# Kernel optimization log

Hardware: AMD Instinct MI355X
Metric: run time of the kernel (lower is better)

## Reference

```python
import jax, jax.numpy as jnp
import numpy as np

B, H, S, D = 4, 32, 2048, 128  # batch, heads, seq_len, d_head
D_MODEL = H * D


def setup_inputs() -> dict:
    key = jax.random.key(0)
    ks = jax.random.split(key, 6)
    return {
        "query_states": jax.random.normal(ks[0], (B, H, S, D), dtype=jnp.float32),
        "key_states": jax.random.normal(ks[1], (B, H, S, D), dtype=jnp.float32),
        "value_states": jax.random.normal(ks[2], (B, H, S, D), dtype=jnp.float32),
        "local_attn_outputs": jax.random.normal(ks[3], (B, H, S, D), dtype=jnp.float32),
        "balance_factors": jax.random.normal(ks[4], (H,), dtype=jnp.float32),
        "w_o": jax.random.normal(ks[5], (D_MODEL, D_MODEL), dtype=jnp.float32) / np.sqrt(D_MODEL),
    }


def reference(query_states, key_states, value_states, local_attn_outputs, balance_factors, w_o):
    # --- compressive memory from keys/values (elu+1 feature map) ---
    phi_k = jax.nn.elu(key_states) + 1.0                                  # [B,H,S,D]
    memory = jnp.einsum("bhsk,bhsv->bhkv", phi_k, value_states)           # [B,H,D,D]
    normalization = jnp.sum(phi_k, axis=2)                                # [B,H,D]

    # --- retrieval with query feature map, normalized ---
    phi_q = jax.nn.elu(query_states) + 1.0                                # [B,H,S,D]
    retrieved = jnp.einsum("bhsk,bhkv->bhsv", phi_q, memory)              # [B,H,S,D]
    denom = jnp.einsum("bhsk,bhk->bhs", phi_q, normalization)             # [B,H,S]
    retrieved = retrieved / denom[..., None]

    # --- sigmoid-gated combine of global (memory) and local attention ---
    gw = jax.nn.sigmoid(balance_factors)[None, :, None, None]             # global weights
    lw = jax.nn.sigmoid(1.0 - balance_factors)[None, :, None, None]      # local weights
    attn = gw * retrieved + lw * local_attn_outputs                       # [B,H,S,D]

    # [B,H,S,D] -> [B,S,H*D]
    attn = jnp.transpose(attn, (0, 2, 1, 3)).reshape(B, S, H * D)
    # o_proj: bias-free Linear, y = x @ W^T
    return attn @ w_o.T
```

## Files before the change

### kernel.cpp

```cpp
#include <hip/hip_runtime.h>
#include <hip/hip_bf16.h>

#define B_ 4
#define H_ 32
#define S_ 2048
#define D_ 128
#define DM_ 4096
#define BH_ (B_*H_)
#define M_ (B_*S_)

typedef short bf16x8 __attribute__((ext_vector_type(8)));
typedef short s16x4  __attribute__((ext_vector_type(4)));
typedef float f32x4  __attribute__((ext_vector_type(4)));

__device__ __forceinline__ float phi_f(float x) {
    return x > 0.f ? x + 1.f : __expf(x);
}

__device__ __forceinline__ short f2b(float x) {
    __hip_bfloat16 h = __float2bfloat16(x);
    return *(short*)&h;
}

__device__ __forceinline__ void gl_lds16(void* lds_uniform, const void* gptr) {
    __builtin_amdgcn_global_load_lds(
        (const __attribute__((address_space(1))) void*)gptr,
        (__attribute__((address_space(3))) void*)lds_uniform,
        16, 0, 0);
}

__global__ __launch_bounds__(256) void k1_memory(
    const float* __restrict__ Kin, const float* __restrict__ Vin,
    float* __restrict__ parts, float* __restrict__ nrm)
{
    const int split = blockIdx.x;
    const int bh = blockIdx.y;
    const int t = threadIdx.x;
    const int wave = t >> 6, lane = t & 63;
    const int lm = lane & 15, quad = lane >> 4;
    const int wm = wave >> 1, wn = wave & 1;

    __shared__ __hip_bfloat16 sVt[128*72];
    __shared__ __hip_bfloat16 sKt[128*72];

    const long base = (long)bh * S_ * D_ + (long)split * (S_/4) * D_;
    const float* Kp = Kin + base;
    const float* Vp = Vin + base;

    f32x4 acc[4][4];
#pragma unroll
    for (int i = 0; i < 4; ++i)
#pragma unroll
        for (int j = 0; j < 4; ++j) { f32x4 z = {0.f,0.f,0.f,0.f}; acc[i][j] = z; }

    float na[2][4] = {{0.f,0.f,0.f,0.f},{0.f,0.f,0.f,0.f}};

    const int si  = t & 15;
    const int dj0 = t >> 4;

    for (int c = 0; c < 8; ++c) {
        const int s0 = c*64 + si*4;
        __syncthreads();
#pragma unroll
        for (int m = 0; m < 2; ++m) {
            const int dj = dj0 + 16*m;
            const float* gK = Kp + (long)s0*D_ + dj*4;
            const float* gV = Vp + (long)s0*D_ + dj*4;
            float4 krv[4], vrv[4];
#pragma unroll
            for (int r = 0; r < 4; ++r) {
                krv[r] = *(const float4*)(gK + (long)r*D_);
                vrv[r] = *(const float4*)(gV + (long)r*D_);
            }
            const float* kf = (const float*)krv;
            const float* vf = (const float*)vrv;
#pragma unroll
            for (int cc = 0; cc < 4; ++cc) {
                float p0 = phi_f(kf[0*4+cc]), p1 = phi_f(kf[1*4+cc]);
                float p2 = phi_f(kf[2*4+cc]), p3 = phi_f(kf[3*4+cc]);
                na[m][cc] += p0 + p1 + p2 + p3;
                s16x4 pw; pw[0]=f2b(p0); pw[1]=f2b(p1); pw[2]=f2b(p2); pw[3]=f2b(p3);
                s16x4 vw; vw[0]=f2b(vf[0*4+cc]); vw[1]=f2b(vf[1*4+cc]);
                          vw[2]=f2b(vf[2*4+cc]); vw[3]=f2b(vf[3*4+cc]);
                const int d = dj*4 + cc;
                *(s16x4*)(sKt + d*72 + si*4) = pw;
                *(s16x4*)(sVt + d*72 + si*4) = vw;
            }
        }
        __syncthreads();
#pragma unroll
        for (int kh = 0; kh < 2; ++kh) {
            const int scol = kh*32 + quad*8;
            bf16x8 af[4], bfr[4];
#pragma unroll
            for (int x = 0; x < 4; ++x) {
                af[x]  = *(const bf16x8*)(sVt + (wm*64 + x*16 + lm)*72 + scol);
                bfr[x] = *(const bf16x8*)(sKt + (wn*64 + x*16 + lm)*72 + scol);
            }
#pragma unroll
            for (int mt = 0; mt < 4; ++mt)
#pragma unroll
                for (int nt = 0; nt < 4; ++nt)
                    acc[mt][nt] = __builtin_amdgcn_mfma_f32_16x16x32_bf16(
                        af[mt], bfr[nt], acc[mt][nt], 0, 0, 0);
        }
    }

#pragma unroll
    for (int m = 0; m < 2; ++m)
#pragma unroll
        for (int cc = 0; cc < 4; ++cc) {
            float v = na[m][cc];
            v += __shfl_xor(v, 1); v += __shfl_xor(v, 2);
            v += __shfl_xor(v, 4); v += __shfl_xor(v, 8);
            if (si == 0)
                atomicAdd(&nrm[bh*D_ + (dj0 + 16*m)*4 + cc], v);
        }

    float* mp = parts + ((long)split*BH_ + bh) * (D_*D_);
#pragma unroll
    for (int mt = 0; mt < 4; ++mt)
#pragma unroll
        for (int nt = 0; nt < 4; ++nt) {
            const int kcol = wn*64 + nt*16 + lm;
#pragma unroll
            for (int r = 0; r < 4; ++r) {
                const int vrow = wm*64 + mt*16 + quad*4 + r;
                mp[vrow*D_ + kcol] = acc[mt][nt][r];
            }
        }
}

__global__ __launch_bounds__(256) void k1b_finalize(
    const float* __restrict__ parts, __hip_bfloat16* __restrict__ memTb)
{
    const long g = (long)blockIdx.x*256 + threadIdx.x;
    const int bh  = (int)(g >> 11);
    const int rem = (int)(g & 2047);
    const int row = rem >> 4, seg = rem & 15;
    const int srcSeg = seg ^ (row & 15);
    const long sbase = (long)bh*(D_*D_) + row*D_ + srcSeg*8;

    f32x4 s0 = {0.f,0.f,0.f,0.f}, s1 = {0.f,0.f,0.f,0.f};
#pragma unroll
    for (int sp = 0; sp < 4; ++sp) {
        const float* p = parts + (long)sp*BH_*(D_*D_) + sbase;
        s0 += *(const f32x4*)p;
        s1 += *(const f32x4*)(p + 4);
    }
    bf16x8 ob;
#pragma unroll
    for (int j = 0; j < 4; ++j) { ob[j] = f2b(s0[j]); ob[4+j] = f2b(s1[j]); }
    *(bf16x8*)(memTb + g*8) = ob;
}

__global__ __launch_bounds__(256) void k2_retrieve(
    const float* __restrict__ Qin, const float* __restrict__ Lin,
    const float* __restrict__ bal,
    const __hip_bfloat16* __restrict__ memTb, const float* __restrict__ nrm,
    __hip_bfloat16* __restrict__ attnB)
{
    const int sc = blockIdx.x;
    const int bh = blockIdx.y;
    const int b = bh >> 5, h = bh & 31;
    const int t = threadIdx.x;
    const int wave = t >> 6, lane = t & 63;
    const int lm = lane & 15, quad = lane >> 4;
    const int wm = wave >> 1, wn = wave & 1;

    __shared__ char smem[128*132*4];
    __hip_bfloat16* sQ = (__hip_bfloat16*)smem;
    __hip_bfloat16* sM = (__hip_bfloat16*)(smem + 32768);
    float* sOut = (float*)smem;
    __shared__ float sDen[128];

    const float* Qp = Qin + (long)bh*S_*D_ + (long)sc*128*D_;
    const float* Lp = Lin + (long)bh*S_*D_ + (long)sc*128*D_;
    const __hip_bfloat16* mb = memTb + (long)bh*(D_*D_);

#pragma unroll
    for (int i = 0; i < 8; ++i)
        gl_lds16((void*)(sM + (i*256 + wave*64)*8),
                 (const void*)(mb + (long)(i*256 + wave*64 + lane)*8));

    const int kq = t & 31;
    const float4 nq = *(const float4*)(nrm + bh*D_ + kq*4);
#pragma unroll
    for (int i = 0; i < 16; ++i) {
        const int idx = t + i*256;
        const int row = idx >> 5;
        float4 qv = *(const float4*)(Qp + (long)idx*4);
        float p0 = phi_f(qv.x), p1 = phi_f(qv.y), p2 = phi_f(qv.z), p3 = phi_f(qv.w);
        float part = p0*nq.x + p1*nq.y + p2*nq.z + p3*nq.w;
        part += __shfl_xor(part, 1);  part += __shfl_xor(part, 2);
        part += __shfl_xor(part, 4);  part += __shfl_xor(part, 8);
        part += __shfl_xor(part, 16);
        if (kq == 0) sDen[row] = part;
        const int seg = kq >> 1, half = kq & 1;
        const int off = row*128 + ((seg ^ (row & 15)) << 3) + half*4;
        s16x4 qw; qw[0]=f2b(p0); qw[1]=f2b(p1); qw[2]=f2b(p2); qw[3]=f2b(p3);
        *(s16x4*)(sQ + off) = qw;
    }
    __syncthreads();

    f32x4 acc[4][4];
#pragma unroll
    for (int i = 0; i < 4; ++i)
#pragma unroll
        for (int j = 0; j < 4; ++j) { f32x4 z = {0.f,0.f,0.f,0.f}; acc[i][j] = z; }

#pragma unroll
    for (int kh = 0; kh < 4; ++kh) {
        const int segk = kh*4 + quad;
        bf16x8 af[4], bfr[4];
#pragma unroll
        for (int x = 0; x < 4; ++x) {
            const int srow = wm*64 + x*16 + lm;
            af[x]  = *(const bf16x8*)(sQ + srow*128 + ((segk ^ (srow & 15)) << 3));
            const int vrow = wn*64 + x*16 + lm;
            bfr[x] = *(const bf16x8*)(sM + vrow*128 + ((segk ^ (vrow & 15)) << 3));
        }
#pragma unroll
        for (int mt = 0; mt < 4; ++mt)
#pragma unroll
            for (int nt = 0; nt < 4; ++nt)
                acc[mt][nt] = __builtin_amdgcn_mfma_f32_16x16x32_bf16(
                    af[mt], bfr[nt], acc[mt][nt], 0, 0, 0);
    }

    const float bv = bal[h];
    const float gw = 1.f/(1.f+__expf(-bv));
    const float lw = 1.f/(1.f+__expf(-(1.f-bv)));

    __syncthreads();
#pragma unroll
    for (int mt = 0; mt < 4; ++mt)
#pragma unroll
        for (int r = 0; r < 4; ++r) {
            const int srow = wm*64 + mt*16 + quad*4 + r;
            const float scale = gw / sDen[srow];
#pragma unroll
            for (int nt = 0; nt < 4; ++nt)
                sOut[srow*132 + wn*64 + nt*16 + lm] = acc[mt][nt][r]*scale;
        }
    __syncthreads();

    const int seg = t & 15;
#pragma unroll
    for (int i = 0; i < 8; ++i) {
        const int row = (t >> 4) + i*16;
        const float* Lr = Lp + (long)row*D_ + seg*8;
        const float* Or = sOut + row*132 + seg*8;
        float4 l0 = *(const float4*)Lr;
        float4 l1 = *(const float4*)(Lr + 4);
        f32x4 o0 = *(const f32x4*)Or;
        f32x4 o1 = *(const f32x4*)(Or + 4);
        bf16x8 ob;
        ob[0] = f2b(o0[0] + lw*l0.x); ob[1] = f2b(o0[1] + lw*l0.y);
        ob[2] = f2b(o0[2] + lw*l0.z); ob[3] = f2b(o0[3] + lw*l0.w);
        ob[4] = f2b(o1[0] + lw*l1.x); ob[5] = f2b(o1[1] + lw*l1.y);
        ob[6] = f2b(o1[2] + lw*l1.z); ob[7] = f2b(o1[3] + lw*l1.w);
        const long oidx = ((long)b*S_ + sc*128 + row)*DM_ + h*D_ + seg*8;
        *(bf16x8*)(attnB + oidx) = ob;
    }
}

__global__ __launch_bounds__(256) void kconv(
    const float* __restrict__ w, __hip_bfloat16* __restrict__ wb)
{
    long i = ((long)blockIdx.x*256 + threadIdx.x)*4;
    float4 f = *(const float4*)(w + i);
    __hip_bfloat16 ob[4] = {__float2bfloat16(f.x), __float2bfloat16(f.y),
                            __float2bfloat16(f.z), __float2bfloat16(f.w)};
    *(uint2*)(wb + i) = *(uint2*)ob;
}

#define GBM 256
#define GBN 256
#define GBK 64
#define GNT (DM_/GBK)

__device__ __forceinline__ bf16x8 ldfrag(const __hip_bfloat16* base, int row, int k) {
    const int kk = k ^ ((row & 7) << 3);
    return *(const bf16x8*)(base + row * GBK + kk);
}

__device__ __forceinline__ void stage_tile(
    const __hip_bfloat16* __restrict__ X, const __hip_bfloat16* __restrict__ W,
    __hip_bfloat16* sAb, __hip_bfloat16* sBb,
    int m0, int n0, int kb, int wave, int lane)
{
#pragma unroll
    for (int r = 0; r < 4; ++r) {
        const int c   = r * 512 + wave * 64 + lane;
        const int row = c >> 3;
        const int ko  = ((c & 7) ^ (row & 7)) * 8;
        gl_lds16((void*)(sAb + (r * 512 + wave * 64) * 8),
                 (const void*)(X + (long)(m0 + row) * DM_ + kb + ko));
    }
#pragma unroll
    for (int r = 0; r < 4; ++r) {
        const int c   = r * 512 + wave * 64 + lane;
        const int row = c >> 3;
        const int ko  = ((c & 7) ^ (row & 7)) * 8;
        gl_lds16((void*)(sBb + (r * 512 + wave * 64) * 8),
                 (const void*)(W + (long)(n0 + row) * DM_ + kb + ko));
    }
}

__global__ __launch_bounds__(512, 2) void k3_gemm(
    const __hip_bfloat16* __restrict__ X,
    const __hip_bfloat16* __restrict__ W,
    float* __restrict__ Y)
{
    __shared__ alignas(16) __hip_bfloat16 sA[2][GBM * GBK];
    __shared__ alignas(16) __hip_bfloat16 sB[2][GBN * GBK];

    const int tid = threadIdx.x;
    const int wave = tid >> 6, lane = tid & 63;
    const int lm = lane & 15, quad = lane >> 4;
    const int wm = wave >> 2, wn = wave & 3;

    const int orig = blockIdx.x;
    const int wg = (orig & 7) * 64 + (orig >> 3);
    const int m0 = (wg >> 4) * GBM;
    const int n0 = (wg & 15) * GBN;

    f32x4 acc[8][4];
#pragma unroll
    for (int i = 0; i < 8; ++i)
#pragma unroll
        for (int j = 0; j < 4; ++j) { f32x4 z = {0.f,0.f,0.f,0.f}; acc[i][j] = z; }

    const int ar0 = wm * 128 + lm;
    const int br0 = wn * 64 + lm;
    const int kq  = quad * 8;

    stage_tile(X, W, sA[0], sB[0], m0, n0, 0, wave, lane);
    stage_tile(X, W, sA[1], sB[1], m0, n0, GBK, wave, lane);
    asm volatile("s_waitcnt vmcnt(8)" ::: "memory");
    __builtin_amdgcn_s_barrier();

    bf16x8 a[4][2], b[4][2];

    for (int t = 0; t < GNT; ++t) {
        const int cur = t & 1;
        const __hip_bfloat16* As = sA[cur];
        const __hip_bfloat16* Bs = sB[cur];

#pragma unroll
        for (int mf = 0; mf < 4; ++mf)
#pragma unroll
            for (int kh = 0; kh < 2; ++kh)
                a[mf][kh] = ldfrag(As, ar0 + mf * 16, kh * 32 + kq);
#pragma unroll
        for (int nf = 0; nf < 2; ++nf)
#pragma unroll
            for (int kh = 0; kh < 2; ++kh)
                b[nf][kh] = ldfrag(Bs, br0 + nf * 16, kh * 32 + kq);
        __builtin_amdgcn_s_barrier();
        asm volatile("s_waitcnt lgkmcnt(0)" ::: "memory");
        __builtin_amdgcn_sched_barrier(0);
        __builtin_amdgcn_s_setprio(1);
#pragma unroll
        for (int mf = 0; mf < 4; ++mf)
#pragma unroll
            for (int nf = 0; nf < 2; ++nf)
#pragma unroll
                for (int kh = 0; kh < 2; ++kh)
                    acc[mf][nf] = __builtin_amdgcn_mfma_f32_16x16x32_bf16(
                        a[mf][kh], b[nf][kh], acc[mf][nf], 0, 0, 0);
        __builtin_amdgcn_s_setprio(0);
        __builtin_amdgcn_s_barrier();

#pragma unroll
        for (int nf = 2; nf < 4; ++nf)
#pragma unroll
            for (int kh = 0; kh < 2; ++kh)
                b[nf][kh] = ldfrag(Bs, br0 + nf * 16, kh * 32 + kq);
        __builtin_amdgcn_s_barrier();
        asm volatile("s_waitcnt lgkmcnt(0)" ::: "memory");
        __builtin_amdgcn_sched_barrier(0);
        __builtin_amdgcn_s_setprio(1);
#pragma unroll
        for (int mf = 0; mf < 4; ++mf)
#pragma unroll
            for (int nf = 2; nf < 4; ++nf)
#pragma unroll
                for (int kh = 0; kh < 2; ++kh)
                    acc[mf][nf] = __builtin_amdgcn_mfma_f32_16x16x32_bf16(
                        a[mf][kh], b[nf][kh], acc[mf][nf], 0, 0, 0);
        __builtin_amdgcn_s_setprio(0);
        __builtin_amdgcn_s_barrier();

#pragma unroll
        for (int mf = 0; mf < 4; ++mf)
#pragma unroll
            for (int kh = 0; kh < 2; ++kh)
                a[mf][kh] = ldfrag(As, ar0 + 64 + mf * 16, kh * 32 + kq);
        __builtin_amdgcn_s_barrier();
        asm volatile("s_waitcnt lgkmcnt(0)" ::: "memory");
        __builtin_amdgcn_sched_barrier(0);
        __builtin_amdgcn_s_setprio(1);
#pragma unroll
        for (int mf = 0; mf < 4; ++mf)
#pragma unroll
            for (int nf = 0; nf < 2; ++nf)
#pragma unroll
                for (int kh = 0; kh < 2; ++kh)
                    acc[4 + mf][nf] = __builtin_amdgcn_mfma_f32_16x16x32_bf16(
                        a[mf][kh], b[nf][kh], acc[4 + mf][nf], 0, 0, 0);
        __builtin_amdgcn_s_setprio(0);
        __builtin_amdgcn_s_barrier();

        if (t + 2 < GNT)
            stage_tile(X, W, sA[cur], sB[cur], m0, n0, (t + 2) * GBK, wave, lane);
        __builtin_amdgcn_s_barrier();
        __builtin_amdgcn_s_setprio(1);
#pragma unroll
        for (int mf = 0; mf < 4; ++mf)
#pragma unroll
            for (int nf = 2; nf < 4; ++nf)
#pragma unroll
                for (int kh = 0; kh < 2; ++kh)
                    acc[4 + mf][nf] = __builtin_amdgcn_mfma_f32_16x16x32_bf16(
                        a[mf][kh], b[nf][kh], acc[4 + mf][nf], 0, 0, 0);
        __builtin_amdgcn_s_setprio(0);
        if (t + 2 < GNT)
            asm volatile("s_waitcnt vmcnt(8)" ::: "memory");
        else
            asm volatile("s_waitcnt vmcnt(0)" ::: "memory");
        __builtin_amdgcn_s_barrier();
    }

#pragma unroll
    for (int mf = 0; mf < 8; ++mf) {
        const int row = m0 + wm * 128 + mf * 16 + quad * 4;
#pragma unroll
        for (int nf = 0; nf < 4; ++nf) {
            const int col = n0 + wn * 64 + nf * 16 + lm;
#pragma unroll
            for (int r = 0; r < 4; ++r)
                Y[(long)(row + r) * DM_ + col] = acc[mf][nf][r];
        }
    }
}

extern "C" void kernel_launch(void* const* d_in, const int* in_sizes, int n_in,
                              void* d_out, int out_size, void* d_ws, size_t ws_size,
                              hipStream_t stream) {
    const float* Q   = (const float*)d_in[0];
    const float* K   = (const float*)d_in[1];
    const float* V   = (const float*)d_in[2];
    const float* L   = (const float*)d_in[3];
    const float* bal = (const float*)d_in[4];
    const float* Wo  = (const float*)d_in[5];
    float* Y = (float*)d_out;

    char* ws = (char*)d_ws;
    float* parts = (float*)ws;
    __hip_bfloat16* woB = (__hip_bfloat16*)ws;
    float* nrm   = (float*)(ws + 33554432);
    __hip_bfloat16* memTb = (__hip_bfloat16*)(ws + 33619968);
    __hip_bfloat16* attnB = (__hip_bfloat16*)(ws + 37814272);

    hipMemsetAsync(nrm, 0, 65536, stream);

    k1_memory<<<dim3(4, BH_), 256, 0, stream>>>(K, V, parts, nrm);
    k1b_finalize<<<1024, 256, 0, stream>>>(parts, memTb);
    kconv<<<DM_*DM_/4/256, 256, 0, stream>>>(Wo, woB);
    k2_retrieve<<<dim3(S_/128, BH_), 256, 0, stream>>>(Q, L, bal, memTb, nrm, attnB);
    k3_gemm<<<dim3(512), 512, 0, stream>>>(attnB, woB, Y);
}
```

Before: 889.6 us.

## Split memory build 8 ways, shorten denominator shuffle, stage GEMM operands separately

The K/V memory accumulation now splits the sequence into 8 chunks instead of 4, doubling the block count for occupancy at the cost of a larger partial buffer and more reads in finalize. The workspace layout is rearranged so the larger partials fit. The retrieval denominator reduction replaces the 5-step shuffle with 2 shuffles plus an LDS partial sum. The GEMM prefetch is split so W tiles are issued earlier than X tiles, spreading global loads across the K-loop phases.

```diff
diff --git a/kernel.cpp b/kernel.cpp
--- a/kernel.cpp
+++ b/kernel.cpp
@@ -43,7 +43,7 @@
     __shared__ __hip_bfloat16 sVt[128*72];
     __shared__ __hip_bfloat16 sKt[128*72];
 
-    const long base = (long)bh * S_ * D_ + (long)split * (S_/4) * D_;
+    const long base = (long)bh * S_ * D_ + (long)split * (S_/8) * D_;
     const float* Kp = Kin + base;
     const float* Vp = Vin + base;
 
@@ -58,7 +58,7 @@
     const int si  = t & 15;
     const int dj0 = t >> 4;
 
-    for (int c = 0; c < 8; ++c) {
+    for (int c = 0; c < 4; ++c) {
         const int s0 = c*64 + si*4;
         __syncthreads();
 #pragma unroll
@@ -143,7 +143,7 @@
 
     f32x4 s0 = {0.f,0.f,0.f,0.f}, s1 = {0.f,0.f,0.f,0.f};
 #pragma unroll
-    for (int sp = 0; sp < 4; ++sp) {
+    for (int sp = 0; sp < 8; ++sp) {
         const float* p = parts + (long)sp*BH_*(D_*D_) + sbase;
         s0 += *(const f32x4*)p;
         s1 += *(const f32x4*)(p + 4);
@@ -172,6 +172,7 @@
     __hip_bfloat16* sQ = (__hip_bfloat16*)smem;
     __hip_bfloat16* sM = (__hip_bfloat16*)(smem + 32768);
     float* sOut = (float*)smem;
+    __shared__ float sDenP[128][8];
     __shared__ float sDen[128];
 
     const float* Qp = Qin + (long)bh*S_*D_ + (long)sc*128*D_;
@@ -192,16 +193,22 @@
         float4 qv = *(const float4*)(Qp + (long)idx*4);
         float p0 = phi_f(qv.x), p1 = phi_f(qv.y), p2 = phi_f(qv.z), p3 = phi_f(qv.w);
         float part = p0*nq.x + p1*nq.y + p2*nq.z + p3*nq.w;
-        part += __shfl_xor(part, 1);  part += __shfl_xor(part, 2);
-        part += __shfl_xor(part, 4);  part += __shfl_xor(part, 8);
-        part += __shfl_xor(part, 16);
-        if (kq == 0) sDen[row] = part;
+        part += __shfl_xor(part, 1);
+        part += __shfl_xor(part, 2);
+        if ((kq & 3) == 0) sDenP[row][kq >> 2] = part;
         const int seg = kq >> 1, half = kq & 1;
         const int off = row*128 + ((seg ^ (row & 15)) << 3) + half*4;
         s16x4 qw; qw[0]=f2b(p0); qw[1]=f2b(p1); qw[2]=f2b(p2); qw[3]=f2b(p3);
         *(s16x4*)(sQ + off) = qw;
     }
     __syncthreads();
+
+    if (t < 128) {
+        float d = 0.f;
+#pragma unroll
+        for (int j = 0; j < 8; ++j) d += sDenP[t][j];
+        sDen[t] = d;
+    }
 
     f32x4 acc[4][4];
 #pragma unroll
@@ -285,26 +292,17 @@
     return *(const bf16x8*)(base + row * GBK + kk);
 }
 
-__device__ __forceinline__ void stage_tile(
-    const __hip_bfloat16* __restrict__ X, const __hip_bfloat16* __restrict__ W,
-    __hip_bfloat16* sAb, __hip_bfloat16* sBb,
-    int m0, int n0, int kb, int wave, int lane)
+__device__ __forceinline__ void stage_half(
+    const __hip_bfloat16* __restrict__ G, __hip_bfloat16* sb,
+    int r0g, int kb, int wave, int lane)
 {
 #pragma unroll
     for (int r = 0; r < 4; ++r) {
         const int c   = r * 512 + wave * 64 + lane;
         const int row = c >> 3;
         const int ko  = ((c & 7) ^ (row & 7)) * 8;
-        gl_lds16((void*)(sAb + (r * 512 + wave * 64) * 8),
-                 (const void*)(X + (long)(m0 + row) * DM_ + kb + ko));
-    }
-#pragma unroll
-    for (int r = 0; r < 4; ++r) {
-        const int c   = r * 512 + wave * 64 + lane;
-        const int row = c >> 3;
-        const int ko  = ((c & 7) ^ (row & 7)) * 8;
-        gl_lds16((void*)(sBb + (r * 512 + wave * 64) * 8),
-                 (const void*)(W + (long)(n0 + row) * DM_ + kb + ko));
+        gl_lds16((void*)(sb + (r * 512 + wave * 64) * 8),
+                 (const void*)(G + (long)(r0g + row) * DM_ + kb + ko));
     }
 }
 
@@ -336,8 +334,10 @@
     const int br0 = wn * 64 + lm;
     const int kq  = quad * 8;
 
-    stage_tile(X, W, sA[0], sB[0], m0, n0, 0, wave, lane);
-    stage_tile(X, W, sA[1], sB[1], m0, n0, GBK, wave, lane);
+    stage_half(W, sB[0], n0, 0, wave, lane);
+    stage_half(X, sA[0], m0, 0, wave, lane);
+    stage_half(W, sB[1], n0, GBK, wave, lane);
+    stage_half(X, sA[1], m0, GBK, wave, lane);
     asm volatile("s_waitcnt vmcnt(8)" ::: "memory");
     __builtin_amdgcn_s_barrier();
 
@@ -393,6 +393,8 @@
         __builtin_amdgcn_s_setprio(0);
         __builtin_amdgcn_s_barrier();
 
+        if (t + 2 < GNT)
+            stage_half(W, sB[cur], n0, (t + 2) * GBK, wave, lane);
 #pragma unroll
         for (int mf = 0; mf < 4; ++mf)
 #pragma unroll
@@ -414,7 +416,7 @@
         __builtin_amdgcn_s_barrier();
 
         if (t + 2 < GNT)
-            stage_tile(X, W, sA[cur], sB[cur], m0, n0, (t + 2) * GBK, wave, lane);
+            stage_half(X, sA[cur], m0, (t + 2) * GBK, wave, lane);
         __builtin_amdgcn_s_barrier();
         __builtin_amdgcn_s_setprio(1);
 #pragma unroll
@@ -459,14 +461,14 @@
 
     char* ws = (char*)d_ws;
     float* parts = (float*)ws;
-    __hip_bfloat16* woB = (__hip_bfloat16*)ws;
-    float* nrm   = (float*)(ws + 33554432);
-    __hip_bfloat16* memTb = (__hip_bfloat16*)(ws + 33619968);
-    __hip_bfloat16* attnB = (__hip_bfloat16*)(ws + 37814272);
+    __hip_bfloat16* attnB = (__hip_bfloat16*)ws;
+    __hip_bfloat16* woB = (__hip_bfloat16*)(ws + 67108864);
+    float* nrm   = (float*)(ws + 100663296);
+    __hip_bfloat16* memTb = (__hip_bfloat16*)(ws + 100728832);
 
     hipMemsetAsync(nrm, 0, 65536, stream);
 
-    k1_memory<<<dim3(4, BH_), 256, 0, stream>>>(K, V, parts, nrm);
+    k1_memory<<<dim3(8, BH_), 256, 0, stream>>>(K, V, parts, nrm);
     k1b_finalize<<<1024, 256, 0, stream>>>(parts, memTb);
     kconv<<<DM_*DM_/4/256, 256, 0, stream>>>(Wo, woB);
     k2_retrieve<<<dim3(S_/128, BH_), 256, 0, stream>>>(Q, L, bal, memTb, nrm, attnB);
```

Result: faster. 829.1 us (-6.8%).
